# Kernel optimization log

Hardware: AMD Instinct MI355X
Metric: run time of the kernel (lower is better)

The kernel has to match this reference:

```python
import jax, jax.numpy as jnp
import numpy as np

N_NODES = 50000


def gcn_conv(x, W, b, src, dst):
    # PyG GCNConv: h = x @ W; add self-loops; norm = deg^{-1/2}[src]*deg^{-1/2}[dst];
    # out = scatter_add(norm * h[src] -> dst) + bias
    h = x @ W  # [N, out]
    ones = jnp.ones(src.shape[0], dtype=x.dtype)
    deg = jax.ops.segment_sum(ones, dst, num_segments=N_NODES) + 1.0  # +1 for self-loop
    inv_sqrt = deg ** -0.5
    norm = inv_sqrt[src] * inv_sqrt[dst]  # [E]
    msgs = h[src] * norm[:, None]  # [E, out]
    agg = jax.ops.segment_sum(msgs, dst, num_segments=N_NODES)
    # self-loop contribution: norm_ii = deg_i^{-1}
    agg = agg + h * (inv_sqrt * inv_sqrt)[:, None]
    return agg + b


def setup_inputs() -> dict:
    key = jax.random.key(0)
    k1, k2, k3, k4 = jax.random.split(key, 4)
    d_in, d_h = 256, 256
    x = jax.random.normal(k1, (N_NODES, d_in), dtype=jnp.float32)
    edge_index = jax.random.randint(k2, (2, 800000), 0, N_NODES, dtype=jnp.int64)
    # Glorot-style params (GCNConv linear has no bias; separate bias added post-agg)
    W1 = jax.random.normal(k3, (d_in, d_h), dtype=jnp.float32) / np.sqrt(d_in)
    W2 = jax.random.normal(k4, (d_h, d_h), dtype=jnp.float32) / np.sqrt(d_h)
    b1 = jnp.zeros((d_h,), dtype=jnp.float32)
    b2 = jnp.zeros((d_h,), dtype=jnp.float32)
    return {"x": x, "edge_index": edge_index, "W1": W1, "b1": b1, "W2": W2, "b2": b2}


def reference(x, edge_index, W1, b1, W2, b2):
    src, dst = edge_index[0], edge_index[1]
    h = jax.nn.relu(gcn_conv(x, W1, b1, src, dst))
    h = jax.nn.relu(gcn_conv(h, W2, b2, src, dst))
    # global_mean_pool with batch=arange(N) assigns each node its own graph -> identity
    return h
```

## Files before the change

kernel.cpp:

```cpp
#include <hip/hip_runtime.h>
#include <hip/hip_bf16.h>

typedef unsigned short u16;
typedef unsigned int u32;

#define N_NODES 50000
#define N_EDGES 800000
#define DHID 256
#define ELLW 64

typedef __attribute__((ext_vector_type(8))) _Float16 f16x8;
typedef __attribute__((ext_vector_type(4))) float f32x4;
typedef __attribute__((ext_vector_type(2))) float f32x2;

__device__ __forceinline__ u16 f2bf(float f) {
    u32 u = __float_as_uint(f);
    u32 r = (u + 0x7FFFu + ((u >> 16) & 1u)) >> 16;
    return (u16)r;
}
__device__ __forceinline__ u16 f2h(float f) {
    _Float16 h = (_Float16)f;
    union { _Float16 h; u16 u; } c; c.h = h;
    return c.u;
}
__device__ __forceinline__ void gl_lds16(const void* g, void* l) {
    __builtin_amdgcn_global_load_lds(
        (const __attribute__((address_space(1))) u32*)g,
        (__attribute__((address_space(3))) u32*)l, 16, 0, 0);
}

#define SPLIT_BLKS 12500
#define ZERO_BLKS 196
__global__ void prep_fused(const float* __restrict__ x, u16* __restrict__ xf,
                           const float* __restrict__ W1, const float* __restrict__ W2,
                           u16* __restrict__ W1t, u16* __restrict__ W2t,
                           int* __restrict__ deg, u32* __restrict__ hszero) {
    const int b = blockIdx.x, tid = threadIdx.x;
    if (b < SPLIT_BLKS) {
        int i = b * 256 + tid;
        float4 v = ((const float4*)x)[i];
        u16 h0 = f2h(v.x), h1 = f2h(v.y), h2 = f2h(v.z), h3 = f2h(v.w);
        uint2 hv;
        hv.x = (u32)h0 | ((u32)h1 << 16);
        hv.y = (u32)h2 | ((u32)h3 << 16);
        ((uint2*)xf)[i] = hv;
    } else if (b < SPLIT_BLKS + ZERO_BLKS) {
        int j = (b - SPLIT_BLKS) * 256 + tid;
        if (j < N_NODES) deg[j] = 0;
        if (j < 128) hszero[j] = 0;
    } else {
        int idx = b - (SPLIT_BLKS + ZERO_BLKS);
        int y = idx >> 8, n = idx & 255, k = tid;
        const float* W = y ? W2 : W1;
        u16* o = y ? W2t : W1t;
        o[n * 256 + k] = f2h(W[k * 256 + n]);
    }
}

__global__ void fill_kernel(const int* __restrict__ src, const int* __restrict__ dst,
                            int* __restrict__ deg, u16* __restrict__ col16, int E) {
    int e = blockIdx.x * 256 + threadIdx.x;
    if (e < E) {
        int d = dst[e];
        int p = atomicAdd(&deg[d], 1);
        if (p < ELLW) col16[(size_t)d * ELLW + p] = (u16)src[e];
    }
}

__global__ __launch_bounds__(256) void gemm_f16_kernel(
    const u16* __restrict__ Af, const u16* __restrict__ Bt,
    const int* __restrict__ deg, u16* __restrict__ out, int M) {
    __shared__ u16 As[128 * 32];
    __shared__ u16 Bs[128 * 32];
    const int tid = threadIdx.x;
    const int wave = tid >> 6;
    const int lane = tid & 63;
    const int wm = wave >> 1, wn = wave & 1;
    const int quad = lane >> 4, l16 = lane & 15;
    const int m0 = blockIdx.x * 128;
    const int n0 = blockIdx.y * 128;

    f32x4 acc[4][4] = {};

    const int row0 = tid >> 2, row1 = (256 + tid) >> 2;
    const int kk = (tid & 3) * 8;
    int ar0 = m0 + row0; if (ar0 >= M) ar0 = M - 1;
    int ar1 = m0 + row1; if (ar1 >= M) ar1 = M - 1;
    const size_t aoff0 = (size_t)ar0 * 256 + kk;
    const size_t aoff1 = (size_t)ar1 * 256 + kk;
    const size_t boff0 = (size_t)(n0 + row0) * 256 + kk;
    const size_t boff1 = (size_t)(n0 + row1) * 256 + kk;
    const size_t l0 = (size_t)(wave * 64) * 8;
    const size_t l1 = (size_t)(256 + wave * 64) * 8;

    for (int ko = 0; ko < 8; ++ko) {
        const int koff = ko * 32;
        __syncthreads();
        gl_lds16(Af + aoff0 + koff, &As[l0]);
        gl_lds16(Af + aoff1 + koff, &As[l1]);
        gl_lds16(Bt + boff0 + koff, &Bs[l0]);
        gl_lds16(Bt + boff1 + koff, &Bs[l1]);
        asm volatile("s_waitcnt vmcnt(0)" ::: "memory");
        __syncthreads();

        f16x8 af[4], bf[4];
#pragma unroll
        for (int mi = 0; mi < 4; ++mi)
            af[mi] = *(const f16x8*)&As[(wm * 64 + mi * 16 + l16) * 32 + quad * 8];
#pragma unroll
        for (int ni = 0; ni < 4; ++ni)
            bf[ni] = *(const f16x8*)&Bs[(wn * 64 + ni * 16 + l16) * 32 + quad * 8];
#pragma unroll
        for (int mi = 0; mi < 4; ++mi)
#pragma unroll
            for (int ni = 0; ni < 4; ++ni)
                acc[mi][ni] = __builtin_amdgcn_mfma_f32_16x16x32_f16(af[mi], bf[ni], acc[mi][ni], 0, 0, 0);
    }

#pragma unroll
    for (int mi = 0; mi < 4; ++mi) {
#pragma unroll
        for (int r = 0; r < 4; ++r) {
            int row = m0 + wm * 64 + mi * 16 + quad * 4 + r;
            if (row < M) {
                float s = rsqrtf((float)deg[row] + 1.0f);
#pragma unroll
                for (int ni = 0; ni < 4; ++ni) {
                    int c = n0 + wn * 64 + ni * 16 + l16;
                    out[(size_t)row * 256 + c] = f2bf(acc[mi][ni][r] * s);
                }
            }
        }
    }
}

__global__ __launch_bounds__(256) void agg_kernel(
    const u16* __restrict__ hs, const u16* __restrict__ col16,
    const int* __restrict__ deg, const float* __restrict__ bias,
    u16* __restrict__ out_f16, float* __restrict__ out_f,
    int mode, int Nn) {
    const int wave = threadIdx.x >> 6, lane = threadIdx.x & 63;
    const int i = blockIdx.x * 4 + wave;
    if (i >= Nn) return;

    const int cnt = deg[i];
    const size_t ebase = (size_t)i * ELLW;
    int entry = Nn;
    if (lane == 0) entry = i;
    else if (lane - 1 < cnt) entry = (int)col16[ebase + lane - 1];
    int entries = cnt + 1;
    if (entries > 64) entries = 64;
    const int nb = (entries + 3) >> 2;
    const size_t lofs = (size_t)lane * 4;

    f32x2 a01 = {0.f, 0.f}, a23 = {0.f, 0.f};

#define ISSUE(b, x0, x1, x2, x3)                                                \
    {                                                                           \
        int e0 = __builtin_amdgcn_readlane(entry, (b) * 4 + 0);                 \
        int e1 = __builtin_amdgcn_readlane(entry, (b) * 4 + 1);                 \
        int e2 = __builtin_amdgcn_readlane(entry, (b) * 4 + 2);                 \
        int e3 = __builtin_amdgcn_readlane(entry, (b) * 4 + 3);                 \
        x0 = *(const uint2*)(hs + (size_t)e0 * 256 + lofs);                     \
        x1 = *(const uint2*)(hs + (size_t)e1 * 256 + lofs);                     \
        x2 = *(const uint2*)(hs + (size_t)e2 * 256 + lofs);                     \
        x3 = *(const uint2*)(hs + (size_t)e3 * 256 + lofs);                     \
    }
#define ACCUM(v)                                                                \
    {                                                                           \
        f32x2 p0, p1;                                                           \
        p0.x = __uint_as_float(v.x << 16);                                      \
        p0.y = __uint_as_float(v.x & 0xffff0000u);                              \
        p1.x = __uint_as_float(v.y << 16);                                      \
        p1.y = __uint_as_float(v.y & 0xffff0000u);                              \
        a01 += p0; a23 += p1;                                                   \
    }

    uint2 c0, c1, c2, c3, d0, d1, d2, d3, n0v, n1v, n2v, n3v;
    ISSUE(0, c0, c1, c2, c3);
    if (nb > 1) ISSUE(1, d0, d1, d2, d3);
    for (int b = 0; b < nb; ++b) {
        const bool more2 = (b + 2 < nb);
        if (more2) ISSUE(b + 2, n0v, n1v, n2v, n3v);
        ACCUM(c0); ACCUM(c1); ACCUM(c2); ACCUM(c3);
        c0 = d0; c1 = d1; c2 = d2; c3 = d3;
        d0 = n0v; d1 = n1v; d2 = n2v; d3 = n3v;
    }
    {
        int cap = cnt < ELLW ? cnt : ELLW;
        for (int j = 63; j < cap; ++j) {
            int s = (int)col16[ebase + j];
            uint2 v = *(const uint2*)(hs + (size_t)s * 256 + lofs);
            ACCUM(v);
        }
    }
#undef ISSUE
#undef ACCUM

    const float inv = rsqrtf((float)cnt + 1.0f);
    float4 bb = *(const float4*)(bias + lane * 4);
    float r0 = fmaxf(fmaf(a01.x, inv, bb.x), 0.0f);
    float r1 = fmaxf(fmaf(a01.y, inv, bb.y), 0.0f);
    float r2 = fmaxf(fmaf(a23.x, inv, bb.z), 0.0f);
    float r3 = fmaxf(fmaf(a23.y, inv, bb.w), 0.0f);
    const size_t o = (size_t)i * 256 + lane * 4;
    if (mode == 0) {
        u16 h0 = f2h(r0), h1 = f2h(r1), h2 = f2h(r2), h3 = f2h(r3);
        uint2 w;
        w.x = (u32)h0 | ((u32)h1 << 16);
        w.y = (u32)h2 | ((u32)h3 << 16);
        *(uint2*)(out_f16 + o) = w;
    } else {
        *(float4*)(out_f + o) = make_float4(r0, r1, r2, r3);
    }
}

extern "C" void kernel_launch(void* const* d_in, const int* in_sizes, int n_in,
                              void* d_out, int out_size, void* d_ws, size_t ws_size,
                              hipStream_t stream) {
    const float* x = (const float*)d_in[0];
    const int* ei = (const int*)d_in[1];
    const float* W1 = (const float*)d_in[2];
    const float* b1 = (const float*)d_in[3];
    const float* W2 = (const float*)d_in[4];
    const float* b2 = (const float*)d_in[5];
    float* out = (float*)d_out;

    const int Nn = N_NODES, E = N_EDGES;
    const int* srcp = ei;
    const int* dstp = ei + E;

    u16* Af = (u16*)d_out;

    char* p = (char*)d_ws;
    auto take = [&](size_t bytes) -> void* {
        void* r = (void*)p;
        p += (bytes + 255) & ~(size_t)255;
        return r;
    };
    u16* hs    = (u16*)take((size_t)(Nn + 1) * DHID * 2);
    u16* col16 = (u16*)take((size_t)Nn * ELLW * 2);
    int* deg   = (int*)take((size_t)Nn * 4);
    u16* W1t   = (u16*)take(256 * 256 * 2);
    u16* W2t   = (u16*)take(256 * 256 * 2);

    prep_fused<<<SPLIT_BLKS + ZERO_BLKS + 512, 256, 0, stream>>>(
        x, Af, W1, W2, W1t, W2t, deg, (u32*)(hs + (size_t)Nn * DHID));
    fill_kernel<<<E / 256, 256, 0, stream>>>(srcp, dstp, deg, col16, E);

    const int gm = (Nn + 127) / 128;
    gemm_f16_kernel<<<dim3(gm, 2), 256, 0, stream>>>(Af, W1t, deg, hs, Nn);
    agg_kernel<<<(Nn + 3) / 4, 256, 0, stream>>>(hs, col16, deg, b1, Af, nullptr, 0, Nn);
    gemm_f16_kernel<<<dim3(gm, 2), 256, 0, stream>>>(Af, W2t, deg, hs, Nn);
    agg_kernel<<<(Nn + 3) / 4, 256, 0, stream>>>(hs, col16, deg, b2, nullptr, out, 1, Nn);
}
```

Before: 305.1 us.

## Double-buffer GEMM LDS tiles and XOR-swizzle layout to avoid bank conflicts

The f16 GEMM now uses two LDS buffers so the global-to-LDS load of the next K slice is issued before the MFMA work on the current slice, overlapping memory latency with compute. The LDS column placement is also XOR-swizzled by row on both the store and fragment-read sides to reduce bank conflicts on the fragment reads. This doubles LDS use per block, which may reduce occupancy, and the swizzle must stay consistent between writer and reader.

Measured after the change: 308.5 us. Within noise of the previous version (+1.1%).

```diff
diff --git a/kernel.cpp b/kernel.cpp
--- a/kernel.cpp
+++ b/kernel.cpp
@@ -70,8 +70,8 @@
 __global__ __launch_bounds__(256) void gemm_f16_kernel(
     const u16* __restrict__ Af, const u16* __restrict__ Bt,
     const int* __restrict__ deg, u16* __restrict__ out, int M) {
-    __shared__ u16 As[128 * 32];
-    __shared__ u16 Bs[128 * 32];
+    __shared__ u16 As[2][128 * 32];
+    __shared__ u16 Bs[2][128 * 32];
     const int tid = threadIdx.x;
     const int wave = tid >> 6;
     const int lane = tid & 63;
@@ -82,40 +82,57 @@
 
     f32x4 acc[4][4] = {};
 
-    const int row0 = tid >> 2, row1 = (256 + tid) >> 2;
-    const int kk = (tid & 3) * 8;
-    int ar0 = m0 + row0; if (ar0 >= M) ar0 = M - 1;
-    int ar1 = m0 + row1; if (ar1 >= M) ar1 = M - 1;
+    const int rl = tid >> 2;
+    const int cl = tid & 3;
+    const int kk = ((cl ^ (rl & 3) ^ ((rl >> 2) & 3)) & 3) * 8;
+    int ar0 = m0 + rl; if (ar0 >= M) ar0 = M - 1;
+    int ar1 = m0 + 64 + rl; if (ar1 >= M) ar1 = M - 1;
     const size_t aoff0 = (size_t)ar0 * 256 + kk;
     const size_t aoff1 = (size_t)ar1 * 256 + kk;
-    const size_t boff0 = (size_t)(n0 + row0) * 256 + kk;
-    const size_t boff1 = (size_t)(n0 + row1) * 256 + kk;
-    const size_t l0 = (size_t)(wave * 64) * 8;
-    const size_t l1 = (size_t)(256 + wave * 64) * 8;
-
+    const size_t boff0 = (size_t)(n0 + rl) * 256 + kk;
+    const size_t boff1 = (size_t)(n0 + 64 + rl) * 256 + kk;
+    const size_t l0 = (size_t)wave * 512;
+    const size_t l1 = 2048 + (size_t)wave * 512;
+
+    const int qs8 = ((quad ^ (l16 & 3) ^ ((l16 >> 2) & 3)) & 3) * 8;
+
+#define STAGE(buf, ko)                                      \
+    {                                                       \
+        const int koff_ = (ko) * 32;                        \
+        gl_lds16(Af + aoff0 + koff_, &As[buf][l0]);         \
+        gl_lds16(Af + aoff1 + koff_, &As[buf][l1]);         \
+        gl_lds16(Bt + boff0 + koff_, &Bs[buf][l0]);         \
+        gl_lds16(Bt + boff1 + koff_, &Bs[buf][l1]);         \
+    }
+
+    STAGE(0, 0);
+    asm volatile("s_waitcnt vmcnt(0)" ::: "memory");
+    __syncthreads();
+
+    int cur = 0;
     for (int ko = 0; ko < 8; ++ko) {
-        const int koff = ko * 32;
-        __syncthreads();
-        gl_lds16(Af + aoff0 + koff, &As[l0]);
-        gl_lds16(Af + aoff1 + koff, &As[l1]);
-        gl_lds16(Bt + boff0 + koff, &Bs[l0]);
-        gl_lds16(Bt + boff1 + koff, &Bs[l1]);
-        asm volatile("s_waitcnt vmcnt(0)" ::: "memory");
-        __syncthreads();
+        if (ko < 7) STAGE(cur ^ 1, ko + 1);
 
         f16x8 af[4], bf[4];
 #pragma unroll
         for (int mi = 0; mi < 4; ++mi)
-            af[mi] = *(const f16x8*)&As[(wm * 64 + mi * 16 + l16) * 32 + quad * 8];
+            af[mi] = *(const f16x8*)&As[cur][(wm * 64 + mi * 16 + l16) * 32 + qs8];
 #pragma unroll
         for (int ni = 0; ni < 4; ++ni)
-            bf[ni] = *(const f16x8*)&Bs[(wn * 64 + ni * 16 + l16) * 32 + quad * 8];
+            bf[ni] = *(const f16x8*)&Bs[cur][(wn * 64 + ni * 16 + l16) * 32 + qs8];
 #pragma unroll
         for (int mi = 0; mi < 4; ++mi)
 #pragma unroll
             for (int ni = 0; ni < 4; ++ni)
                 acc[mi][ni] = __builtin_amdgcn_mfma_f32_16x16x32_f16(af[mi], bf[ni], acc[mi][ni], 0, 0, 0);
-    }
+
+        if (ko < 7) {
+            asm volatile("s_waitcnt vmcnt(0)" ::: "memory");
+            __syncthreads();
+            cur ^= 1;
+        }
+    }
+#undef STAGE
 
 #pragma unroll
     for (int mi = 0; mi < 4; ++mi) {
```

## Fuse edge fill into prep kernel and make GEMM load fragments directly

Applied to the files above, without the earlier changes.

The edge-fill pass (degree atomics plus ELL column writes) moves into the prep kernel as extra blocks, each handling four edges per thread. Zeroing of the degree counts goes to a small separate kernel launched first. The GEMM drops its LDS staging and barriers: each wave loads its own A and B fragments straight from global memory and computes a 64x128 tile, with a 256-row block tile and a launch bound that asks for two blocks per CU. This cuts launches and synchronisation, at the cost of more register pressure and repeated global loads of B with no LDS sharing between waves.

After: 329.2 us. 7.9% more time.

```diff
diff --git a/kernel.cpp b/kernel.cpp
--- a/kernel.cpp
+++ b/kernel.cpp
@@ -23,18 +23,21 @@
     union { _Float16 h; u16 u; } c; c.h = h;
     return c.u;
 }
-__device__ __forceinline__ void gl_lds16(const void* g, void* l) {
-    __builtin_amdgcn_global_load_lds(
-        (const __attribute__((address_space(1))) u32*)g,
-        (__attribute__((address_space(3))) u32*)l, 16, 0, 0);
+
+__global__ void zero_kernel(int* __restrict__ deg, u32* __restrict__ hs32) {
+    int j = blockIdx.x * 256 + threadIdx.x;
+    if (j < N_NODES) deg[j] = 0;
+    if (j < 128) hs32[(size_t)N_NODES * 128 + j] = 0;
 }
 
 #define SPLIT_BLKS 12500
-#define ZERO_BLKS 196
-__global__ void prep_fused(const float* __restrict__ x, u16* __restrict__ xf,
-                           const float* __restrict__ W1, const float* __restrict__ W2,
-                           u16* __restrict__ W1t, u16* __restrict__ W2t,
-                           int* __restrict__ deg, u32* __restrict__ hszero) {
+#define W_BLKS 512
+#define FILL_BLKS 782
+__global__ void prep_fill(const float* __restrict__ x, u16* __restrict__ xf,
+                          const float* __restrict__ W1, const float* __restrict__ W2,
+                          u16* __restrict__ W1t, u16* __restrict__ W2t,
+                          const int* __restrict__ src, const int* __restrict__ dst,
+                          int* __restrict__ deg, u16* __restrict__ col16) {
     const int b = blockIdx.x, tid = threadIdx.x;
     if (b < SPLIT_BLKS) {
         int i = b * 256 + tid;
@@ -44,90 +47,82 @@
         hv.x = (u32)h0 | ((u32)h1 << 16);
         hv.y = (u32)h2 | ((u32)h3 << 16);
         ((uint2*)xf)[i] = hv;
-    } else if (b < SPLIT_BLKS + ZERO_BLKS) {
-        int j = (b - SPLIT_BLKS) * 256 + tid;
-        if (j < N_NODES) deg[j] = 0;
-        if (j < 128) hszero[j] = 0;
-    } else {
-        int idx = b - (SPLIT_BLKS + ZERO_BLKS);
+    } else if (b < SPLIT_BLKS + W_BLKS) {
+        int idx = b - SPLIT_BLKS;
         int y = idx >> 8, n = idx & 255, k = tid;
         const float* W = y ? W2 : W1;
         u16* o = y ? W2t : W1t;
         o[n * 256 + k] = f2h(W[k * 256 + n]);
-    }
-}
-
-__global__ void fill_kernel(const int* __restrict__ src, const int* __restrict__ dst,
-                            int* __restrict__ deg, u16* __restrict__ col16, int E) {
-    int e = blockIdx.x * 256 + threadIdx.x;
-    if (e < E) {
-        int d = dst[e];
-        int p = atomicAdd(&deg[d], 1);
-        if (p < ELLW) col16[(size_t)d * ELLW + p] = (u16)src[e];
-    }
-}
-
-__global__ __launch_bounds__(256) void gemm_f16_kernel(
+    } else {
+        const int e0 = (b - SPLIT_BLKS - W_BLKS) * 1024 + tid;
+        int ds[4], ps[4], ss[4];
+        bool ok[4];
+#pragma unroll
+        for (int q = 0; q < 4; ++q) {
+            int e = e0 + q * 256;
+            ok[q] = (e < N_EDGES);
+            if (ok[q]) { ds[q] = dst[e]; ss[q] = src[e]; }
+        }
+#pragma unroll
+        for (int q = 0; q < 4; ++q)
+            if (ok[q]) ps[q] = atomicAdd(&deg[ds[q]], 1);
+#pragma unroll
+        for (int q = 0; q < 4; ++q)
+            if (ok[q] && ps[q] < ELLW) col16[(size_t)ds[q] * ELLW + ps[q]] = (u16)ss[q];
+    }
+}
+
+__global__ __launch_bounds__(256, 2) void gemm_f16_kernel(
     const u16* __restrict__ Af, const u16* __restrict__ Bt,
     const int* __restrict__ deg, u16* __restrict__ out, int M) {
-    __shared__ u16 As[128 * 32];
-    __shared__ u16 Bs[128 * 32];
     const int tid = threadIdx.x;
     const int wave = tid >> 6;
     const int lane = tid & 63;
-    const int wm = wave >> 1, wn = wave & 1;
     const int quad = lane >> 4, l16 = lane & 15;
-    const int m0 = blockIdx.x * 128;
+    const int rowbase = blockIdx.x * 256 + wave * 64;
     const int n0 = blockIdx.y * 128;
 
-    f32x4 acc[4][4] = {};
-
-    const int row0 = tid >> 2, row1 = (256 + tid) >> 2;
-    const int kk = (tid & 3) * 8;
-    int ar0 = m0 + row0; if (ar0 >= M) ar0 = M - 1;
-    int ar1 = m0 + row1; if (ar1 >= M) ar1 = M - 1;
-    const size_t aoff0 = (size_t)ar0 * 256 + kk;
-    const size_t aoff1 = (size_t)ar1 * 256 + kk;
-    const size_t boff0 = (size_t)(n0 + row0) * 256 + kk;
-    const size_t boff1 = (size_t)(n0 + row1) * 256 + kk;
-    const size_t l0 = (size_t)(wave * 64) * 8;
-    const size_t l1 = (size_t)(256 + wave * 64) * 8;
-
-    for (int ko = 0; ko < 8; ++ko) {
-        const int koff = ko * 32;
-        __syncthreads();
-        gl_lds16(Af + aoff0 + koff, &As[l0]);
-        gl_lds16(Af + aoff1 + koff, &As[l1]);
-        gl_lds16(Bt + boff0 + koff, &Bs[l0]);
-        gl_lds16(Bt + boff1 + koff, &Bs[l1]);
-        asm volatile("s_waitcnt vmcnt(0)" ::: "memory");
-        __syncthreads();
-
-        f16x8 af[4], bf[4];
-#pragma unroll
-        for (int mi = 0; mi < 4; ++mi)
-            af[mi] = *(const f16x8*)&As[(wm * 64 + mi * 16 + l16) * 32 + quad * 8];
-#pragma unroll
-        for (int ni = 0; ni < 4; ++ni)
-            bf[ni] = *(const f16x8*)&Bs[(wn * 64 + ni * 16 + l16) * 32 + quad * 8];
-#pragma unroll
-        for (int mi = 0; mi < 4; ++mi)
-#pragma unroll
-            for (int ni = 0; ni < 4; ++ni)
-                acc[mi][ni] = __builtin_amdgcn_mfma_f32_16x16x32_f16(af[mi], bf[ni], acc[mi][ni], 0, 0, 0);
-    }
-
-#pragma unroll
-    for (int mi = 0; mi < 4; ++mi) {
+    f32x4 acc[4][8] = {};
+
+    size_t aoff[4];
+#pragma unroll
+    for (int rt = 0; rt < 4; ++rt) {
+        int ar = rowbase + rt * 16 + l16;
+        if (ar >= M) ar = M - 1;
+        aoff[rt] = (size_t)ar * 256 + quad * 8;
+    }
+    size_t boff[8];
+#pragma unroll
+    for (int nt = 0; nt < 8; ++nt)
+        boff[nt] = (size_t)(n0 + nt * 16 + l16) * 256 + quad * 8;
+
+    for (int kt = 0; kt < 8; ++kt) {
+        const int ko = kt * 32;
+        f16x8 bfr[8], afr[4];
+#pragma unroll
+        for (int nt = 0; nt < 8; ++nt)
+            bfr[nt] = *(const f16x8*)&Bt[boff[nt] + ko];
+#pragma unroll
+        for (int rt = 0; rt < 4; ++rt)
+            afr[rt] = *(const f16x8*)&Af[aoff[rt] + ko];
+#pragma unroll
+        for (int rt = 0; rt < 4; ++rt)
+#pragma unroll
+            for (int nt = 0; nt < 8; ++nt)
+                acc[rt][nt] = __builtin_amdgcn_mfma_f32_16x16x32_f16(afr[rt], bfr[nt], acc[rt][nt], 0, 0, 0);
+    }
+
+#pragma unroll
+    for (int rt = 0; rt < 4; ++rt) {
 #pragma unroll
         for (int r = 0; r < 4; ++r) {
-            int row = m0 + wm * 64 + mi * 16 + quad * 4 + r;
+            int row = rowbase + rt * 16 + quad * 4 + r;
             if (row < M) {
                 float s = rsqrtf((float)deg[row] + 1.0f);
 #pragma unroll
-                for (int ni = 0; ni < 4; ++ni) {
-                    int c = n0 + wn * 64 + ni * 16 + l16;
-                    out[(size_t)row * 256 + c] = f2bf(acc[mi][ni][r] * s);
+                for (int nt = 0; nt < 8; ++nt) {
+                    int c = n0 + nt * 16 + l16;
+                    out[(size_t)row * 256 + c] = f2bf(acc[rt][nt][r] * s);
                 }
             }
         }
@@ -244,11 +239,11 @@
     u16* W1t   = (u16*)take(256 * 256 * 2);
     u16* W2t   = (u16*)take(256 * 256 * 2);
 
-    prep_fused<<<SPLIT_BLKS + ZERO_BLKS + 512, 256, 0, stream>>>(
-        x, Af, W1, W2, W1t, W2t, deg, (u32*)(hs + (size_t)Nn * DHID));
-    fill_kernel<<<E / 256, 256, 0, stream>>>(srcp, dstp, deg, col16, E);
-
-    const int gm = (Nn + 127) / 128;
+    zero_kernel<<<196, 256, 0, stream>>>(deg, (u32*)hs);
+    prep_fill<<<SPLIT_BLKS + W_BLKS + FILL_BLKS, 256, 0, stream>>>(
+        x, Af, W1, W2, W1t, W2t, srcp, dstp, deg, col16);
+
+    const int gm = (Nn + 255) / 256;
     gemm_f16_kernel<<<dim3(gm, 2), 256, 0, stream>>>(Af, W1t, deg, hs, Nn);
     agg_kernel<<<(Nn + 3) / 4, 256, 0, stream>>>(hs, col16, deg, b1, Af, nullptr, 0, Nn);
     gemm_f16_kernel<<<dim3(gm, 2), 256, 0, stream>>>(Af, W2t, deg, hs, Nn);
```
